# Optimization experiments

Measured on AMD Instinct MI355X. Metric: run time of the kernel, lower is better.

## Reference

```python
import jax, jax.numpy as jnp
import numpy as np

N_HEADS = 4
D_K = 64
SCALE = D_K ** -0.5


def setup_inputs() -> dict:
    key = jax.random.key(0)
    k1, k2, k3 = jax.random.split(key, 3)
    B, C, S = 8, 256, 2048
    x = jax.random.normal(k1, (B, C, S), dtype=jnp.float32)
    # Linear(C, 3*H*dk): weight [out, in] as in torch
    w_proj = jax.random.normal(k2, (3 * N_HEADS * D_K, C), dtype=jnp.float32) * (C ** -0.5)
    b_proj = jnp.zeros((3 * N_HEADS * D_K,), dtype=jnp.float32)
    w_out = jax.random.normal(k3, (C, N_HEADS * D_K), dtype=jnp.float32) * ((N_HEADS * D_K) ** -0.5)
    b_out = jnp.zeros((C,), dtype=jnp.float32)
    return {"x": x, "w_proj": w_proj, "b_proj": b_proj, "w_out": w_out, "b_out": b_out}


def reference(x, w_proj, b_proj, w_out, b_out):
    B, C, S = x.shape
    xt = jnp.transpose(x, (0, 2, 1))                    # [B, S, C]
    qkv = xt @ w_proj.T + b_proj                        # [B, S, 3*H*dk]
    qkv = qkv.reshape(B, S, N_HEADS, 3 * D_K)
    q, k, v = jnp.split(qkv, 3, axis=-1)                # each [B, S, H, dk]
    attn = jnp.einsum('bihd,bjhd->bijh', q, k) * SCALE  # [B, S, S, H]
    attn = jax.nn.softmax(attn, axis=2)                 # softmax over key axis j
    res = jnp.einsum('bijh,bjhd->bihd', attn, v)        # [B, S, H, dk]
    res = res.reshape(B, S, N_HEADS * D_K)
    res = res @ w_out.T + b_out + xt                    # residual in [B, S, C]
    return jnp.transpose(res, (0, 2, 1))                # back to [B, C, S]
```

## Files before the change

kernel.cpp:

```cpp
#include <hip/hip_runtime.h>


typedef _Float16 f16;
typedef __attribute__((ext_vector_type(4))) float f32x4;
typedef __attribute__((ext_vector_type(8))) _Float16 h8;
typedef __attribute__((ext_vector_type(4))) _Float16 h4;
typedef __attribute__((ext_vector_type(2))) __fp16 fp16x2;
typedef __attribute__((ext_vector_type(4))) __fp16 fp16x4;
typedef __attribute__((ext_vector_type(8))) __fp16 fp16x8;

#define SS 2048
#define CC 256
#define BB 8
#define HH 4
#define DK 64
#define O3 768
#define NT64 32
#define C1F 0.1803368801111204f
#define C2L2 11.541560327111707f

#define MFMA32(a, b, c) __builtin_amdgcn_mfma_f32_16x16x32_f16(a, b, c, 0, 0, 0)

#if __has_builtin(__builtin_amdgcn_exp2f)
#define EXP2(x) __builtin_amdgcn_exp2f(x)
#else
#define EXP2(x) exp2f(x)
#endif

__device__ __forceinline__ void async_ld16(const f16* g, f16* lds) {
  __builtin_amdgcn_global_load_lds(
      (const __attribute__((address_space(1))) unsigned int*)g,
      (__attribute__((address_space(3))) unsigned int*)lds, 16, 0, 0);
}

__global__ __launch_bounds__(256) void k_prep(const float* __restrict__ x,
                                              f16* __restrict__ xt,
                                              const float* __restrict__ w_proj,
                                              const float* __restrict__ w_out,
                                              f16* __restrict__ wp, f16* __restrict__ wo) {
  if (blockIdx.z == 8) {
    int slice = blockIdx.y * 32 + blockIdx.x;
    int i0 = slice * 2048 + threadIdx.x * 8;
    const float* src;
    f16* dst;
    if (i0 < O3 * CC) {
      src = w_proj + i0;
      int row = i0 >> 8, ch = (i0 & 255) >> 3;
      dst = wp + row * 256 + ((ch ^ (row & 7)) << 3);
    } else {
      int j = i0 - O3 * CC;
      src = w_out + j;
      int row = j >> 8, ch = (j & 255) >> 3;
      dst = wo + row * 256 + ((ch ^ (row & 7)) << 3);
    }
    float4 a = *(const float4*)src;
    float4 b = *(const float4*)(src + 4);
    h8 v = {(f16)a.x, (f16)a.y, (f16)a.z, (f16)a.w,
            (f16)b.x, (f16)b.y, (f16)b.z, (f16)b.w};
    *(h8*)dst = v;
    return;
  }
  __shared__ float tile[64][65];
  int b = blockIdx.z, c0 = blockIdx.y * 64, s0 = blockIdx.x * 64;
  int t = threadIdx.x;
#pragma unroll
  for (int it = 0; it < 16; ++it) {
    int idx = it * 256 + t;
    int cl = idx >> 6, sl = idx & 63;
    tile[cl][sl] = x[(size_t)(b * CC + c0 + cl) * SS + s0 + sl];
  }
  __syncthreads();
#pragma unroll
  for (int cid = t; cid < 512; cid += 256) {
    int sl = cid >> 3, chl = cid & 7;
    int s = s0 + sl;
    int gch = (c0 >> 3) + chl;
    h8 v;
#pragma unroll
    for (int e = 0; e < 8; ++e) v[e] = (f16)tile[chl * 8 + e][sl];
    *(h8*)(xt + (size_t)(b * SS + s) * CC + ((gch ^ (s & 7)) << 3)) = v;
  }
}

__global__ __launch_bounds__(256) void k_qkv(const f16* __restrict__ xt,
                                             const f16* __restrict__ wp,
                                             const float* __restrict__ bp,
                                             f16* __restrict__ qh, f16* __restrict__ ksw,
                                             f16* __restrict__ vsw) {
  __shared__ f16 As[16384];
  __shared__ f16 Bs[16384];
  __shared__ f16 Ot[4096];
  int b = blockIdx.z;
  int oti = blockIdx.y, o0 = oti * 64;
  int s0 = blockIdx.x * 64;
  int w = threadIdx.x >> 6, l = threadIdx.x & 63;
  int lr = l & 15, lg = l >> 4;

  const f16* Ag = xt + ((size_t)b * SS + s0) * CC;
  const f16* Bg = wp + (size_t)o0 * CC;
#pragma unroll
  for (int i = 0; i < 8; ++i) {
    int off = w * 4096 + i * 512;
    async_ld16(Ag + off + l * 8, &As[off]);
    async_ld16(Bg + off + l * 8, &Bs[off]);
  }
  asm volatile("s_waitcnt vmcnt(0)" ::: "memory");
  __syncthreads();

  f32x4 acc[4] = {};
#pragma unroll
  for (int kk = 0; kk < CC; kk += 32) {
    int chs = (((kk >> 3) + lg) ^ (lr & 7)) << 3;
    h8 af = *(const h8*)&As[(w * 16 + lr) * 256 + chs];
#pragma unroll
    for (int n = 0; n < 4; ++n) {
      h8 bf = *(const h8*)&Bs[(n * 16 + lr) * 256 + chs];
      acc[n] = MFMA32(af, bf, acc[n]);
    }
  }

  int seg = oti % 3;
  int h = oti / 3;
  int bh = b * HH + h;
  float scl = (seg == 0) ? C1F : 1.0f;
#pragma unroll
  for (int n = 0; n < 4; ++n) {
    float bb = bp[o0 + n * 16 + lr];
#pragma unroll
    for (int r = 0; r < 4; ++r) acc[n][r] = (acc[n][r] + bb) * scl;
  }

  if (seg == 2) {
#pragma unroll
    for (int n = 0; n < 4; ++n) {
      int d = n * 16 + lr;
#pragma unroll
      for (int r = 0; r < 4; ++r) {
        int sl = w * 16 + lg * 4 + r;
        int kl = sl & 31;
        int ps = ((kl & 15) >> 2) ^ ((d >> 1) & 3);
        Ot[(sl >> 5) * 2048 + d * 32 + ps * 8 + ((kl >> 4) << 2) + (kl & 3)] =
            (f16)acc[n][r];
      }
    }
  } else if (seg == 1) {
#pragma unroll
    for (int n = 0; n < 4; ++n) {
      int d = n * 16 + lr;
#pragma unroll
      for (int r = 0; r < 4; ++r) {
        int sl = w * 16 + lg * 4 + r;
        int kl = sl & 31;
        Ot[(sl >> 5) * 2048 + kl * 64 + (((d >> 3) ^ (kl & 7)) << 3) + (d & 7)] =
            (f16)acc[n][r];
      }
    }
  } else {
#pragma unroll
    for (int n = 0; n < 4; ++n)
#pragma unroll
      for (int r = 0; r < 4; ++r)
        Ot[(w * 16 + lg * 4 + r) * 64 + n * 16 + lr] = (f16)acc[n][r];
  }
  __syncthreads();

  int t = threadIdx.x;
  f16* dst;
  if (seg == 0)
    dst = qh + ((size_t)bh * SS + s0) * DK;
  else if (seg == 1)
    dst = ksw + ((size_t)bh * NT64 + (s0 >> 6)) * 4096;
  else
    dst = vsw + ((size_t)bh * NT64 + (s0 >> 6)) * 4096;
  *(int4*)(dst + t * 16) = *(const int4*)&Ot[t * 16];
  *(int4*)(dst + t * 16 + 8) = *(const int4*)&Ot[t * 16 + 8];
}

__global__ __launch_bounds__(256, 3) void k_attn(const f16* __restrict__ qh,
                                                 const f16* __restrict__ ksw,
                                                 const f16* __restrict__ vsw,
                                                 f16* __restrict__ res) {
  __shared__ f16 kbuf[2][4096];
  __shared__ f16 vbuf[2][4096];
  int id = blockIdx.x;
  int xcd = id & 7, slot = id >> 3;
  int bh = xcd * 4 + (slot >> 4);
  int qt = slot & 15;
  int w = threadIdx.x >> 6, l = threadIdx.x & 63;
  int qg = w & 1, kg = w >> 1;
  int q0w = qt * 128 + qg * 64;
  int lr = l & 15, lg = l >> 4;

  h8 qf[4][2];
#pragma unroll
  for (int qs = 0; qs < 4; ++qs) {
    const f16* qp = qh + (size_t)(bh * SS + q0w + qs * 16 + lr) * DK;
    qf[qs][0] = *(const h8*)(qp + lg * 8);
    qf[qs][1] = *(const h8*)(qp + 32 + lg * 8);
  }

  const f16* kg_ = ksw + (size_t)bh * (SS * DK);
  const f16* vg_ = vsw + (size_t)bh * (SS * DK);

#define STAGE(bufi, tile)                                            \
  {                                                                  \
    const f16* kq = kg_ + (size_t)(tile) * 4096 + w * 1024 + l * 8;  \
    const f16* vq = vg_ + (size_t)(tile) * 4096 + w * 1024 + l * 8;  \
    f16* kd = &kbuf[bufi][w * 1024];                                 \
    f16* vd = &vbuf[bufi][w * 1024];                                 \
    async_ld16(kq, kd);                                              \
    async_ld16(kq + 512, kd + 512);                                  \
    async_ld16(vq, vd);                                              \
    async_ld16(vq + 512, vd + 512);                                  \
  }

  int swk = (lr & 7) << 3;
  int ek[2][2];
#pragma unroll
  for (int kb = 0; kb < 2; ++kb)
#pragma unroll
    for (int ch = 0; ch < 2; ++ch)
      ek[kb][ch] = (lr + kb * 16) * 64 + ((ch * 32 + lg * 8) ^ swk);
  int ev = lr * 32 + ((lg ^ ((lr >> 1) & 3)) * 8);

  f32x4 oacc[4][4] = {};
  float dsum[4] = {0.f, 0.f, 0.f, 0.f};
  const f32x4 cinit = {-C2L2, -C2L2, -C2L2, -C2L2};

  int sb = kg * 2048;

  STAGE(0, 0);
  STAGE(1, 1);

  for (int kt = 0; kt < NT64; ++kt) {
    int cur = kt & 1;
    asm volatile("s_waitcnt vmcnt(4)" ::: "memory");
    __builtin_amdgcn_sched_barrier(0);
    __builtin_amdgcn_s_barrier();
    __builtin_amdgcn_sched_barrier(0);

    const f16* kb_ = &kbuf[cur][sb];
    const f16* vb_ = &vbuf[cur][sb];
    h8 kf[2][2];
#pragma unroll
    for (int kb = 0; kb < 2; ++kb)
#pragma unroll
      for (int ch = 0; ch < 2; ++ch) kf[kb][ch] = *(const h8*)&kb_[ek[kb][ch]];
    h8 vv[4];
#pragma unroll
    for (int m = 0; m < 4; ++m) vv[m] = *(const h8*)&vb_[ev + m * 512];

    __builtin_amdgcn_s_setprio(1);
#pragma unroll
    for (int qs = 0; qs < 4; ++qs) {
      f32x4 sacc[2];
#pragma unroll
      for (int kb = 0; kb < 2; ++kb) {
        sacc[kb] = MFMA32(kf[kb][0], qf[qs][0], cinit);
        sacc[kb] = MFMA32(kf[kb][1], qf[qs][1], sacc[kb]);
      }
      float e0 = EXP2(sacc[0][0]);
      float e1 = EXP2(sacc[0][1]);
      float e2 = EXP2(sacc[0][2]);
      float e3 = EXP2(sacc[0][3]);
      float e4 = EXP2(sacc[1][0]);
      float e5 = EXP2(sacc[1][1]);
      float e6 = EXP2(sacc[1][2]);
      float e7 = EXP2(sacc[1][3]);
      dsum[qs] += ((e0 + e1) + (e2 + e3)) + ((e4 + e5) + (e6 + e7));
      fp16x2 p01 = __builtin_amdgcn_cvt_pkrtz(e0, e1);
      fp16x2 p23 = __builtin_amdgcn_cvt_pkrtz(e2, e3);
      fp16x2 p45 = __builtin_amdgcn_cvt_pkrtz(e4, e5);
      fp16x2 p67 = __builtin_amdgcn_cvt_pkrtz(e6, e7);
      fp16x4 lo4 = __builtin_shufflevector(p01, p23, 0, 1, 2, 3);
      fp16x4 hi4 = __builtin_shufflevector(p45, p67, 0, 1, 2, 3);
      fp16x8 p8 = __builtin_shufflevector(lo4, hi4, 0, 1, 2, 3, 4, 5, 6, 7);
      h8 pf8 = __builtin_bit_cast(h8, p8);
#pragma unroll
      for (int m = 0; m < 4; ++m) oacc[qs][m] = MFMA32(vv[m], pf8, oacc[qs][m]);
    }
    __builtin_amdgcn_s_setprio(0);

    __builtin_amdgcn_sched_barrier(0);
    __builtin_amdgcn_s_barrier();
    __builtin_amdgcn_sched_barrier(0);
    int nxt = (kt + 2) & (NT64 - 1);
    STAGE(cur, nxt);
  }

#pragma unroll
  for (int qs = 0; qs < 4; ++qs) {
    dsum[qs] += __shfl_xor(dsum[qs], 16, 64);
    dsum[qs] += __shfl_xor(dsum[qs], 32, 64);
  }

  asm volatile("s_waitcnt vmcnt(0)" ::: "memory");
  __syncthreads();

  float* red = (float*)&kbuf[0][0];
  float* redd = (float*)&vbuf[0][0];
  if (kg == 1) {
#pragma unroll
    for (int qs = 0; qs < 4; ++qs) redd[(qg * 4 + qs) * 64 + l] = dsum[qs];
  }
  int b = bh >> 2, h = bh & 3;
#pragma unroll
  for (int half = 0; half < 2; ++half) {
    if (kg == 1) {
#pragma unroll
      for (int q2 = 0; q2 < 2; ++q2)
#pragma unroll
        for (int m = 0; m < 4; ++m)
          *(f32x4*)&red[((qg * 2 + q2) * 4 + m) * 256 + l * 4] =
              oacc[half * 2 + q2][m];
    }
    __syncthreads();
    if (kg == 0) {
#pragma unroll
      for (int q2 = 0; q2 < 2; ++q2) {
        int qs = half * 2 + q2;
        float inv = 1.0f / (dsum[qs] + redd[(qg * 4 + qs) * 64 + l]);
        int s = q0w + qs * 16 + lr;
        f16* rrow = res + (size_t)(b * SS + s) * CC;
        int sk = s & 7;
#pragma unroll
        for (int m = 0; m < 4; ++m) {
          f32x4 o2 = *(const f32x4*)&red[((qg * 2 + q2) * 4 + m) * 256 + l * 4];
          int d = h * 64 + m * 16 + lg * 4;
          int ch = d >> 3;
          h4 rv;
#pragma unroll
          for (int r = 0; r < 4; ++r) rv[r] = (f16)((oacc[qs][m][r] + o2[r]) * inv);
          *(h4*)(rrow + ((ch ^ sk) << 3) + (d & 7)) = rv;
        }
      }
    }
    __syncthreads();
  }
}

__global__ __launch_bounds__(256) void k_out(const f16* __restrict__ res,
                                             const f16* __restrict__ wo,
                                             const float* __restrict__ bo,
                                             const float* __restrict__ x,
                                             float* __restrict__ out) {
  __shared__ f16 As[16384];
  __shared__ f16 Bs[16384];
  __shared__ float Xs[4096];
  float* Ot = (float*)As;

  int b = blockIdx.z;
  int c0 = blockIdx.y * 64;
  int s0 = blockIdx.x * 64;
  int w = threadIdx.x >> 6, l = threadIdx.x & 63;
  int lr = l & 15, lg = l >> 4;

  const f16* Ag = res + ((size_t)b * SS + s0) * CC;
  const f16* Bg = wo + (size_t)c0 * CC;
#pragma unroll
  for (int i = 0; i < 8; ++i) {
    int off = w * 4096 + i * 512;
    async_ld16(Ag + off + l * 8, &As[off]);
    async_ld16(Bg + off + l * 8, &Bs[off]);
  }
#pragma unroll
  for (int i = 0; i < 4; ++i) {
    int cl = w * 16 + i * 4 + (l >> 4);
    int cidx = l & 15;
    const float* src =
        x + ((size_t)b * CC + c0 + cl) * SS + s0 + ((cidx ^ (cl & 7)) << 2);
    async_ld16((const f16*)src, (f16*)&Xs[w * 1024 + i * 256 + l * 4]);
  }
  asm volatile("s_waitcnt vmcnt(0)" ::: "memory");
  __syncthreads();

  f32x4 acc[4] = {};
#pragma unroll
  for (int kk = 0; kk < CC; kk += 32) {
    int chs = (((kk >> 3) + lg) ^ (lr & 7)) << 3;
    h8 af = *(const h8*)&As[(w * 16 + lr) * 256 + chs];
#pragma unroll
    for (int n = 0; n < 4; ++n) {
      h8 bf = *(const h8*)&Bs[(n * 16 + lr) * 256 + chs];
      acc[n] = MFMA32(af, bf, acc[n]);
    }
  }
  __syncthreads();

#pragma unroll
  for (int n = 0; n < 4; ++n) {
    int c = c0 + n * 16 + lr;
    float bb = bo[c];
    float4 xv =
        *(const float4*)&Xs[(n * 16 + lr) * 64 + (((w * 4 + lg) ^ (lr & 7)) << 2)];
    float4 ov;
    ov.x = acc[n][0] + bb + xv.x;
    ov.y = acc[n][1] + bb + xv.y;
    ov.z = acc[n][2] + bb + xv.z;
    ov.w = acc[n][3] + bb + xv.w;
    *(float4*)&Ot[(n * 16 + lr) * 68 + w * 16 + lg * 4] = ov;
  }
  __syncthreads();

  int cl = threadIdx.x >> 2, sc = (threadIdx.x & 3) * 16;
  float* orow = out + ((size_t)b * CC + c0 + cl) * SS + s0 + sc;
  const float* srow = &Ot[cl * 68 + sc];
#pragma unroll
  for (int j = 0; j < 4; ++j) *(float4*)(orow + j * 4) = *(const float4*)(srow + j * 4);
}

extern "C" void kernel_launch(void* const* d_in, const int* in_sizes, int n_in,
                              void* d_out, int out_size, void* d_ws, size_t ws_size,
                              hipStream_t stream) {
  const float* x = (const float*)d_in[0];
  const float* w_proj = (const float*)d_in[1];
  const float* b_proj = (const float*)d_in[2];
  const float* w_out = (const float*)d_in[3];
  const float* b_out = (const float*)d_in[4];
  float* out = (float*)d_out;

  char* p = (char*)d_ws;
  f16* xt = (f16*)p; p += (size_t)BB * SS * CC * 2;
  f16* wp = (f16*)p; p += (size_t)O3 * CC * 2;
  f16* wo = (f16*)p; p += (size_t)CC * CC * 2;
  f16* qh = (f16*)p; p += (size_t)BB * HH * SS * DK * 2;
  f16* ksw = (f16*)p; p += (size_t)BB * HH * SS * DK * 2;
  f16* vsw = (f16*)p; p += (size_t)BB * HH * SS * DK * 2;
  f16* res = (f16*)p;

  k_prep<<<dim3(SS / 64, CC / 64, BB + 1), 256, 0, stream>>>(x, xt, w_proj, w_out, wp, wo);
  k_qkv<<<dim3(SS / 64, O3 / 64, BB), 256, 0, stream>>>(xt, wp, b_proj, qh, ksw, vsw);
  k_attn<<<dim3(512), 256, 0, stream>>>(qh, ksw, vsw, res);
  k_out<<<dim3(SS / 64, CC / 64, BB), 256, 0, stream>>>(res, wo, b_out, x, out);
}
```

Baseline: 86.84 us.

## Shrink attention blocks to two waves over 64 queries, doubling grid size

The attention kernel moves from 256-thread blocks (two query groups by two key groups) to 128-thread blocks with one 64-query tile split across two key-split waves, and the grid doubles to 1024 blocks. Each wave now stages twice as much K/V per tile, and the wait count changes to match. The split-K reduction collapses into a single pass. The aim is finer-grained blocks for better load balance and occupancy. The cost is that each K/V tile loaded into LDS is reused by half as many query rows, which doubles global K/V traffic per query.

Result: no change. 87.38 us (+0.6%).

```diff
diff --git a/kernel.cpp b/kernel.cpp
--- a/kernel.cpp
+++ b/kernel.cpp
@@ -176,7 +176,7 @@
   *(int4*)(dst + t * 16 + 8) = *(const int4*)&Ot[t * 16 + 8];
 }
 
-__global__ __launch_bounds__(256, 3) void k_attn(const f16* __restrict__ qh,
+__global__ __launch_bounds__(128, 2) void k_attn(const f16* __restrict__ qh,
                                                  const f16* __restrict__ ksw,
                                                  const f16* __restrict__ vsw,
                                                  f16* __restrict__ res) {
@@ -184,11 +184,11 @@
   __shared__ f16 vbuf[2][4096];
   int id = blockIdx.x;
   int xcd = id & 7, slot = id >> 3;
-  int bh = xcd * 4 + (slot >> 4);
-  int qt = slot & 15;
+  int bh = xcd * 4 + (slot >> 5);
+  int qt = slot & 31;
   int w = threadIdx.x >> 6, l = threadIdx.x & 63;
-  int qg = w & 1, kg = w >> 1;
-  int q0w = qt * 128 + qg * 64;
+  int kg = w;
+  int q0w = qt * 64;
   int lr = l & 15, lg = l >> 4;
 
   h8 qf[4][2];
@@ -199,19 +199,23 @@
     qf[qs][1] = *(const h8*)(qp + 32 + lg * 8);
   }
 
-  const f16* kg_ = ksw + (size_t)bh * (SS * DK);
-  const f16* vg_ = vsw + (size_t)bh * (SS * DK);
+  const f16* kgp = ksw + (size_t)bh * (SS * DK);
+  const f16* vgp = vsw + (size_t)bh * (SS * DK);
 
 #define STAGE(bufi, tile)                                            \
   {                                                                  \
-    const f16* kq = kg_ + (size_t)(tile) * 4096 + w * 1024 + l * 8;  \
-    const f16* vq = vg_ + (size_t)(tile) * 4096 + w * 1024 + l * 8;  \
-    f16* kd = &kbuf[bufi][w * 1024];                                 \
-    f16* vd = &vbuf[bufi][w * 1024];                                 \
+    const f16* kq = kgp + (size_t)(tile) * 4096 + w * 2048 + l * 8;  \
+    const f16* vq = vgp + (size_t)(tile) * 4096 + w * 2048 + l * 8;  \
+    f16* kd = &kbuf[bufi][w * 2048];                                 \
+    f16* vd = &vbuf[bufi][w * 2048];                                 \
     async_ld16(kq, kd);                                              \
     async_ld16(kq + 512, kd + 512);                                  \
+    async_ld16(kq + 1024, kd + 1024);                                \
+    async_ld16(kq + 1536, kd + 1536);                                \
     async_ld16(vq, vd);                                              \
     async_ld16(vq + 512, vd + 512);                                  \
+    async_ld16(vq + 1024, vd + 1024);                                \
+    async_ld16(vq + 1536, vd + 1536);                                \
   }
 
   int swk = (lr & 7) << 3;
@@ -234,7 +238,7 @@
 
   for (int kt = 0; kt < NT64; ++kt) {
     int cur = kt & 1;
-    asm volatile("s_waitcnt vmcnt(4)" ::: "memory");
+    asm volatile("s_waitcnt vmcnt(8)" ::: "memory");
     __builtin_amdgcn_sched_barrier(0);
     __builtin_amdgcn_s_barrier();
     __builtin_amdgcn_sched_barrier(0);
@@ -301,41 +305,33 @@
   float* redd = (float*)&vbuf[0][0];
   if (kg == 1) {
 #pragma unroll
-    for (int qs = 0; qs < 4; ++qs) redd[(qg * 4 + qs) * 64 + l] = dsum[qs];
-  }
-  int b = bh >> 2, h = bh & 3;
-#pragma unroll
-  for (int half = 0; half < 2; ++half) {
-    if (kg == 1) {
-#pragma unroll
-      for (int q2 = 0; q2 < 2; ++q2)
-#pragma unroll
-        for (int m = 0; m < 4; ++m)
-          *(f32x4*)&red[((qg * 2 + q2) * 4 + m) * 256 + l * 4] =
-              oacc[half * 2 + q2][m];
-    }
-    __syncthreads();
-    if (kg == 0) {
-#pragma unroll
-      for (int q2 = 0; q2 < 2; ++q2) {
-        int qs = half * 2 + q2;
-        float inv = 1.0f / (dsum[qs] + redd[(qg * 4 + qs) * 64 + l]);
-        int s = q0w + qs * 16 + lr;
-        f16* rrow = res + (size_t)(b * SS + s) * CC;
-        int sk = s & 7;
-#pragma unroll
-        for (int m = 0; m < 4; ++m) {
-          f32x4 o2 = *(const f32x4*)&red[((qg * 2 + q2) * 4 + m) * 256 + l * 4];
-          int d = h * 64 + m * 16 + lg * 4;
-          int ch = d >> 3;
-          h4 rv;
-#pragma unroll
-          for (int r = 0; r < 4; ++r) rv[r] = (f16)((oacc[qs][m][r] + o2[r]) * inv);
-          *(h4*)(rrow + ((ch ^ sk) << 3) + (d & 7)) = rv;
-        }
+    for (int qs = 0; qs < 4; ++qs) {
+#pragma unroll
+      for (int m = 0; m < 4; ++m)
+        *(f32x4*)&red[(qs * 4 + m) * 256 + l * 4] = oacc[qs][m];
+      redd[qs * 64 + l] = dsum[qs];
+    }
+  }
+  __syncthreads();
+  if (kg == 0) {
+    int b = bh >> 2, h = bh & 3;
+#pragma unroll
+    for (int qs = 0; qs < 4; ++qs) {
+      float inv = 1.0f / (dsum[qs] + redd[qs * 64 + l]);
+      int s = q0w + qs * 16 + lr;
+      f16* rrow = res + (size_t)(b * SS + s) * CC;
+      int sk = s & 7;
+#pragma unroll
+      for (int m = 0; m < 4; ++m) {
+        f32x4 o2 = *(const f32x4*)&red[(qs * 4 + m) * 256 + l * 4];
+        int d = h * 64 + m * 16 + lg * 4;
+        int ch = d >> 3;
+        h4 rv;
+#pragma unroll
+        for (int r = 0; r < 4; ++r) rv[r] = (f16)((oacc[qs][m][r] + o2[r]) * inv);
+        *(h4*)(rrow + ((ch ^ sk) << 3) + (d & 7)) = rv;
       }
     }
-    __syncthreads();
   }
 }
 
@@ -430,6 +426,6 @@
 
   k_prep<<<dim3(SS / 64, CC / 64, BB + 1), 256, 0, stream>>>(x, xt, w_proj, w_out, wp, wo);
   k_qkv<<<dim3(SS / 64, O3 / 64, BB), 256, 0, stream>>>(xt, wp, b_proj, qh, ksw, vsw);
-  k_attn<<<dim3(512), 256, 0, stream>>>(qh, ksw, vsw, res);
+  k_attn<<<dim3(1024), 128, 0, stream>>>(qh, ksw, vsw, res);
   k_out<<<dim3(SS / 64, CC / 64, BB), 256, 0, stream>>>(res, wo, b_out, x, out);
 }
```
